# Kernel tuning notes

Hardware: AMD Instinct MI355X
Metric: run time of the kernel (lower is better)

## Reference

```python
import jax, jax.numpy as jnp
import numpy as np

A = 9  # len(scales) * len(ratios) anchor templates
DN = ('NHWC', 'HWIO', 'NHWC')


def _conv(x, w, b):
    y = jax.lax.conv_general_dilated(x, w, window_strides=(1, 1), padding='SAME',
                                     dimension_numbers=DN)
    return y + b


def setup_inputs() -> dict:
    key = jax.random.key(0)
    ks = jax.random.split(key, 9)
    s = 0.02  # weight init scale
    x = jax.random.normal(ks[0], (4, 128, 128, 512), jnp.float32)
    W1 = jax.random.normal(ks[1], (3, 3, 512, 256), jnp.float32) * s
    b1 = jnp.zeros((256,), jnp.float32)
    W2 = jax.random.normal(ks[2], (3, 3, 256, 256), jnp.float32) * s
    b2 = jnp.zeros((256,), jnp.float32)
    Wr = jax.random.normal(ks[3], (1, 1, 256, 4 * A), jnp.float32) * s
    br = jnp.zeros((4 * A,), jnp.float32)
    Wc = jax.random.normal(ks[4], (1, 1, 256, 2 * A), jnp.float32) * s
    bc = jnp.zeros((2 * A,), jnp.float32)
    return {'x': x, 'W1': W1, 'b1': b1, 'W2': W2, 'b2': b2,
            'Wr': Wr, 'br': br, 'Wc': Wc, 'bc': bc}


def reference(x, W1, b1, W2, b2, Wr, br, Wc, bc):
    h = jax.nn.relu(_conv(x, W1, b1))
    h = jax.nn.relu(_conv(h, W2, b2))
    B, H, W = h.shape[0], h.shape[1], h.shape[2]
    reg = _conv(h, Wr, br).reshape(B, H, W, A, 4)            # (B,H,W,A,4)
    cls = _conv(h, Wc, bc).reshape(B, H, W, A, 2)            # (B,H,W,A,2)
    cls = jax.nn.softmax(cls, axis=4)
    return jnp.concatenate((cls, reg), axis=4)               # (B,H,W,A,6)
```

## Files before the change

kernel.cpp:

```cpp
#include <hip/hip_runtime.h>


typedef float f32x4  __attribute__((ext_vector_type(4)));
typedef float f32x16 __attribute__((ext_vector_type(16)));
typedef short bf16x8 __attribute__((ext_vector_type(8)));

union U16x8 { uint4 v; unsigned short s[8]; };

__device__ __forceinline__ unsigned short f2bf(float f) {
  union { float f; unsigned int u; } v; v.f = f;
  unsigned int r = v.u + 0x7FFFu + ((v.u >> 16) & 1u);
  return (unsigned short)(r >> 16);
}

#define GLOAD_LDS16(G, L)                                        \
  __builtin_amdgcn_global_load_lds(                              \
      (const __attribute__((address_space(1))) void*)(G),        \
      (__attribute__((address_space(3))) void*)(L), 16, 0, 0)

__global__ __launch_bounds__(256) void transpose_cvt(
    const float* __restrict__ src, unsigned short* __restrict__ dst,
    int K, int N) {
  __shared__ float t[32][33];
  const int tx = threadIdx.x, ty = threadIdx.y;
  const int k0 = blockIdx.x * 32, n0 = blockIdx.y * 32;
  const float* s = src + (size_t)blockIdx.z * K * N;
  unsigned short* d = dst + (size_t)blockIdx.z * N * K;
#pragma unroll
  for (int r = 0; r < 32; r += 8) {
    int k = k0 + ty + r, n = n0 + tx;
    t[ty + r][tx] = (k < K && n < N) ? s[(size_t)k * N + n] : 0.f;
  }
  __syncthreads();
#pragma unroll
  for (int r = 0; r < 32; r += 8) {
    int n = n0 + ty + r, k = k0 + tx;
    if (n < N && k < K) d[(size_t)n * K + k] = f2bf(t[tx][ty + r]);
  }
}

__global__ __launch_bounds__(256) void convert_x(
    const float* __restrict__ x, unsigned short* __restrict__ xp) {
  int idx = blockIdx.x * 256 + threadIdx.x;
  int g = idx & 63;
  int cell = idx >> 6;
  int xpix = cell % 130;
  int t = cell / 130;
  int ypix = t % 130;
  int b = t / 130;
  U16x8 u;
  if (xpix == 0 || xpix == 129 || ypix == 0 || ypix == 129) {
    u.v = make_uint4(0u, 0u, 0u, 0u);
  } else {
    const float* sp = x + ((size_t)((b * 128 + ypix - 1) * 128) + (xpix - 1)) * 512 + g * 8;
    float4 a = *(const float4*)sp;
    float4 c = *(const float4*)(sp + 4);
    u.s[0] = f2bf(a.x); u.s[1] = f2bf(a.y); u.s[2] = f2bf(a.z); u.s[3] = f2bf(a.w);
    u.s[4] = f2bf(c.x); u.s[5] = f2bf(c.y); u.s[6] = f2bf(c.z); u.s[7] = f2bf(c.w);
  }
  *(uint4*)(xp + (size_t)cell * 512 + g * 8) = u.v;
}

__global__ __launch_bounds__(256) void zero_h1_borders(unsigned short* __restrict__ h1p) {
  int idx = blockIdx.x * 256 + threadIdx.x;
  int g = idx & 31;
  int cell = idx >> 5;
  int xpix = cell % 130;
  int t = cell / 130;
  int ypix = t % 130;
  if (xpix == 0 || xpix == 129 || ypix == 0 || ypix == 129)
    *(uint4*)(h1p + (size_t)cell * 256 + g * 8) = make_uint4(0u, 0u, 0u, 0u);
}

template<int CIN, int MODE>
__global__ __launch_bounds__(512, 2) void conv3x3(
    const unsigned short* __restrict__ Ap,
    const unsigned short* __restrict__ WT,
    const float* __restrict__ bias,
    unsigned short* __restrict__ out) {
  constexpr int NCI    = CIN / 32;
  constexpr int LOGNCI = (NCI == 16) ? 4 : 3;
  constexpr int NT     = 3 * NCI;
  constexpr int A_BYTES = 2 * 192 * 4 * 16;
  constexpr int B_BYTES = 3 * 256 * 4 * 16;
  constexpr int BUF     = A_BYTES + B_BYTES;
  __shared__ __align__(16) unsigned char smem[2 * BUF];

  const int tid  = threadIdx.x;
  const int wave = tid >> 6, lane = tid & 63;
  const int l31 = lane & 31, hi = lane >> 5;
  const int wm = wave >> 2, wn = wave & 3;
  const int b = blockIdx.x >> 6;
  const int y0 = (blockIdx.x & 63) * 2;
  const int brow = b * 130 + y0;

  int a_go[3], a_ld[3];
#pragma unroll
  for (int i = 0; i < 3; ++i) {
    int s = (wave * 3 + i) * 64 + lane;
    int br = (s >= 768) ? 1 : 0;
    int r = s - br * 768;
    int px = r >> 2, sl = r & 3;
    a_go[i] = (br * 130 + px) * CIN + ((sl ^ ((px >> 1) & 3)) * 8);
    a_ld[i] = (wave * 3 + i) * 1024;
  }
  int b_go[6], b_ld[6];
#pragma unroll
  for (int i = 0; i < 6; ++i) {
    int s = (wave * 6 + i) * 64 + lane;
    int dxs = s >> 10, r = s & 1023;
    int co = r >> 2, sl = r & 3;
    b_go[i] = (dxs * 256 + co) * CIN + ((sl ^ ((co >> 1) & 3)) * 8);
    b_ld[i] = A_BYTES + (wave * 6 + i) * 1024;
  }

  const float bb0 = bias[wn * 64 + l31];
  const float bb1 = bias[wn * 64 + 32 + l31];

  f32x16 acc[4][2] = {};
  const int bswz = (l31 >> 1) & 3;

  auto stage = [&](int tile) {
    const int dy  = tile >> LOGNCI;
    const int ci0 = (tile & (NCI - 1)) << 5;
    unsigned char* sb = smem + (size_t)(tile & 1) * BUF;
    const unsigned short* Ab = Ap + (size_t)(brow + dy) * 130 * CIN + ci0;
#pragma unroll
    for (int i = 0; i < 3; ++i)
      GLOAD_LDS16(Ab + a_go[i], sb + a_ld[i]);
    const unsigned short* Bb = WT + (size_t)dy * 3 * 256 * CIN + ci0;
#pragma unroll
    for (int i = 0; i < 6; ++i)
      GLOAD_LDS16(Bb + b_go[i], sb + b_ld[i]);
  };

  stage(0);
  asm volatile("s_waitcnt vmcnt(0)" ::: "memory");
  __builtin_amdgcn_s_barrier();

#pragma unroll 2
  for (int t = 0; t < NT; ++t) {
    const unsigned char* sb = smem + (size_t)(t & 1) * BUF;
#pragma unroll
    for (int dx = 0; dx < 3; ++dx) {
      const int aswz  = ((l31 + dx) >> 1) & 3;
      const int abase = wm * 12288 + (l31 + dx) * 64;
      const int bbase = A_BYTES + dx * 16384 + wn * 4096 + l31 * 64;
      bf16x8 af[2][4], bfr[2][2];
#pragma unroll
      for (int ks = 0; ks < 2; ++ks) {
        const int q  = ks * 2 + hi;
        const int ab  = abase + ((q ^ aswz) * 16);
        const int bby = bbase + ((q ^ bswz) * 16);
#pragma unroll
        for (int i = 0; i < 4; ++i)
          af[ks][i] = *(const bf16x8*)(sb + ab + i * 2048);
#pragma unroll
        for (int j = 0; j < 2; ++j)
          bfr[ks][j] = *(const bf16x8*)(sb + bby + j * 2048);
      }
      if (dx == 0 && t + 1 < NT) stage(t + 1);
      if (dx == 2 && t + 1 < NT)
        asm volatile("s_waitcnt vmcnt(0)" ::: "memory");
      __builtin_amdgcn_sched_barrier(0);
      __builtin_amdgcn_s_barrier();
      asm volatile("s_waitcnt lgkmcnt(0)" ::: "memory");
      __builtin_amdgcn_sched_barrier(0);
      __builtin_amdgcn_s_setprio(1);
#pragma unroll
      for (int ks = 0; ks < 2; ++ks)
#pragma unroll
        for (int i = 0; i < 4; ++i)
#pragma unroll
          for (int j = 0; j < 2; ++j)
            acc[i][j] = __builtin_amdgcn_mfma_f32_32x32x16_bf16(
                af[ks][i], bfr[ks][j], acc[i][j], 0, 0, 0);
      __builtin_amdgcn_s_setprio(0);
      __builtin_amdgcn_sched_barrier(0);
      __builtin_amdgcn_s_barrier();
    }
  }

#pragma unroll
  for (int i = 0; i < 4; ++i) {
#pragma unroll
    for (int j = 0; j < 2; ++j) {
      const int n = wn * 64 + j * 32 + l31;
      const float bb = j ? bb1 : bb0;
#pragma unroll
      for (int reg = 0; reg < 16; ++reg) {
        int px = i * 32 + (reg & 3) + 8 * (reg >> 2) + 4 * hi;
        float v = fmaxf(acc[i][j][reg] + bb, 0.f);
        size_t off;
        if (MODE == 0)
          off = ((size_t)(brow + wm + 1) * 130 + (px + 1)) * 256 + n;
        else
          off = ((size_t)(b * 128 + y0 + wm) * 128 + px) * 256 + n;
        out[off] = f2bf(v);
      }
    }
  }
}

__global__ __launch_bounds__(256) void heads_kernel(
    const unsigned short* __restrict__ h2,
    const unsigned short* __restrict__ WhT,
    const float* __restrict__ br, const float* __restrict__ bc,
    float* __restrict__ out) {
  __shared__ __align__(16) unsigned short As[64][264];
  const int tid = threadIdx.x;
  const int wave = tid >> 6, lane = tid & 63;
  const int quad = lane >> 4, l16 = lane & 15;
  const int pix0 = blockIdx.x * 64;
#pragma unroll
  for (int r = 0; r < 8; ++r) {
    int s = r * 256 + tid;
    int row = s >> 5, seg = s & 31;
    *(uint4*)&As[row][seg * 8] =
        *(const uint4*)(h2 + (size_t)(pix0 + row) * 256 + seg * 8);
  }
  __syncthreads();
  f32x4 acc[4] = {};
#pragma unroll
  for (int ks = 0; ks < 8; ++ks) {
    bf16x8 af = *(const bf16x8*)&As[wave * 16 + l16][ks * 32 + quad * 8];
#pragma unroll
    for (int j = 0; j < 4; ++j) {
      bf16x8 bfr = *(const bf16x8*)(WhT + (size_t)(j * 16 + l16) * 256 + ks * 32 + quad * 8);
      acc[j] = __builtin_amdgcn_mfma_f32_16x16x32_bf16(af, bfr, acc[j], 0, 0, 0);
    }
  }
#pragma unroll
  for (int j = 0; j < 4; ++j) {
    int n = j * 16 + l16;
    float bias = 0.f;
    if (n < 18) bias = bc[n];
    else if (n < 54) bias = br[n - 18];
#pragma unroll
    for (int r = 0; r < 4; ++r) {
      int p = pix0 + wave * 16 + quad * 4 + r;
      float v = acc[j][r] + bias;
      float partner = __shfl_xor(v, 1);
      if (n < 18) {
        float mx = fmaxf(v, partner);
        float e0 = __expf(v - mx), e1 = __expf(partner - mx);
        int a = n >> 1, sl = n & 1;
        out[(size_t)p * 54 + a * 6 + sl] = e0 / (e0 + e1);
      } else if (n < 54) {
        int rr = n - 18, a = rr >> 2, sl = (rr & 3) + 2;
        out[(size_t)p * 54 + a * 6 + sl] = v;
      }
    }
  }
}

extern "C" void kernel_launch(void* const* d_in, const int* in_sizes, int n_in,
                              void* d_out, int out_size, void* d_ws, size_t ws_size,
                              hipStream_t stream) {
  const float* x  = (const float*)d_in[0];
  const float* W1 = (const float*)d_in[1];
  const float* b1 = (const float*)d_in[2];
  const float* W2 = (const float*)d_in[3];
  const float* b2 = (const float*)d_in[4];
  const float* Wr = (const float*)d_in[5];
  const float* br = (const float*)d_in[6];
  const float* Wc = (const float*)d_in[7];
  const float* bc = (const float*)d_in[8];
  float* out = (float*)d_out;

  constexpr size_t XPAD_B  = 4ull * 130 * 130 * 512 * 2;
  constexpr size_t H1PAD_B = 4ull * 130 * 130 * 256 * 2;
  constexpr size_t H2_B    = 4ull * 128 * 128 * 256 * 2;
  constexpr size_t W1T_B   = 9ull * 256 * 512 * 2;
  constexpr size_t W2T_B   = 9ull * 256 * 256 * 2;
  char* ws = (char*)d_ws;
  unsigned short* x_pad  = (unsigned short*)(ws);
  unsigned short* h1_pad = (unsigned short*)(ws + XPAD_B);
  unsigned short* h2     = (unsigned short*)(ws + XPAD_B + H1PAD_B);
  unsigned short* W1T    = (unsigned short*)(ws + XPAD_B + H1PAD_B + H2_B);
  unsigned short* W2T    = (unsigned short*)(ws + XPAD_B + H1PAD_B + H2_B + W1T_B);
  unsigned short* WhT    = (unsigned short*)(ws + XPAD_B + H1PAD_B + H2_B + W1T_B + W2T_B);

  hipMemsetAsync(WhT, 0, 64ull * 256 * 2, stream);
  transpose_cvt<<<dim3(16, 8, 9), dim3(32, 8), 0, stream>>>(W1, W1T, 512, 256);
  transpose_cvt<<<dim3(8, 8, 9),  dim3(32, 8), 0, stream>>>(W2, W2T, 256, 256);
  transpose_cvt<<<dim3(8, 1, 1),  dim3(32, 8), 0, stream>>>(Wc, WhT, 256, 18);
  transpose_cvt<<<dim3(8, 2, 1),  dim3(32, 8), 0, stream>>>(Wr, WhT + 18 * 256, 256, 36);
  convert_x<<<16900, 256, 0, stream>>>(x, x_pad);
  zero_h1_borders<<<8450, 256, 0, stream>>>(h1_pad);
  conv3x3<512, 0><<<256, 512, 0, stream>>>(x_pad, W1T, b1, h1_pad);
  conv3x3<256, 1><<<256, 512, 0, stream>>>(h1_pad, W2T, b2, h2);
  heads_kernel<<<1024, 256, 0, stream>>>(h2, WhT, br, bc, out);
}
```

Measured before the change: 481.5 us.

## Halve conv workgroup to 4 waves with 128x128 tiles and register-double-buffered fragments

The conv kernel now runs 4 waves per block instead of 8, so each wave owns a 128x128 output tile (16 accumulators) rather than 128x64. This raises MFMA work per LDS fragment load. LDS fragment loads are double-buffered in registers (X/Y sets) and overlapped with MFMAs using partial lgkmcnt waits, and the per-dx barriers are replaced by one barrier per k-tile. In exchange, each wave carries much higher register pressure (256 accumulator floats plus fragments), launch_bounds(256,1) limits occupancy, and each thread issues twice as many global-to-LDS copies.

```diff
diff --git a/kernel.cpp b/kernel.cpp
--- a/kernel.cpp
+++ b/kernel.cpp
@@ -73,7 +73,7 @@
 }
 
 template<int CIN, int MODE>
-__global__ __launch_bounds__(512, 2) void conv3x3(
+__global__ __launch_bounds__(256, 1) void conv3x3(
     const unsigned short* __restrict__ Ap,
     const unsigned short* __restrict__ WT,
     const float* __restrict__ bias,
@@ -89,35 +89,29 @@
   const int tid  = threadIdx.x;
   const int wave = tid >> 6, lane = tid & 63;
   const int l31 = lane & 31, hi = lane >> 5;
-  const int wm = wave >> 2, wn = wave & 3;
+  const int wm = wave >> 1, wn = wave & 1;
   const int b = blockIdx.x >> 6;
   const int y0 = (blockIdx.x & 63) * 2;
   const int brow = b * 130 + y0;
 
-  int a_go[3], a_ld[3];
-#pragma unroll
-  for (int i = 0; i < 3; ++i) {
-    int s = (wave * 3 + i) * 64 + lane;
-    int br = (s >= 768) ? 1 : 0;
-    int r = s - br * 768;
-    int px = r >> 2, sl = r & 3;
-    a_go[i] = (br * 130 + px) * CIN + ((sl ^ ((px >> 1) & 3)) * 8);
-    a_ld[i] = (wave * 3 + i) * 1024;
-  }
-  int b_go[6], b_ld[6];
+  int a_go[6], b_go[12];
 #pragma unroll
   for (int i = 0; i < 6; ++i) {
     int s = (wave * 6 + i) * 64 + lane;
+    int rw = (s >= 768) ? 1 : 0;
+    int r = s - rw * 768;
+    int px = r >> 2, sl = r & 3;
+    a_go[i] = (rw * 130 + px) * CIN + ((sl ^ ((px >> 1) & 3)) * 8);
+  }
+#pragma unroll
+  for (int i = 0; i < 12; ++i) {
+    int s = (wave * 12 + i) * 64 + lane;
     int dxs = s >> 10, r = s & 1023;
     int co = r >> 2, sl = r & 3;
     b_go[i] = (dxs * 256 + co) * CIN + ((sl ^ ((co >> 1) & 3)) * 8);
-    b_ld[i] = A_BYTES + (wave * 6 + i) * 1024;
-  }
-
-  const float bb0 = bias[wn * 64 + l31];
-  const float bb1 = bias[wn * 64 + 32 + l31];
-
-  f32x16 acc[4][2] = {};
+  }
+
+  f32x16 acc[4][4] = {};
   const int bswz = (l31 >> 1) & 3;
 
   auto stage = [&](int tile) {
@@ -126,67 +120,94 @@
     unsigned char* sb = smem + (size_t)(tile & 1) * BUF;
     const unsigned short* Ab = Ap + (size_t)(brow + dy) * 130 * CIN + ci0;
 #pragma unroll
-    for (int i = 0; i < 3; ++i)
-      GLOAD_LDS16(Ab + a_go[i], sb + a_ld[i]);
+    for (int i = 0; i < 6; ++i)
+      GLOAD_LDS16(Ab + a_go[i], sb + (wave * 6 + i) * 1024);
     const unsigned short* Bb = WT + (size_t)dy * 3 * 256 * CIN + ci0;
 #pragma unroll
-    for (int i = 0; i < 6; ++i)
-      GLOAD_LDS16(Bb + b_go[i], sb + b_ld[i]);
+    for (int i = 0; i < 12; ++i)
+      GLOAD_LDS16(Bb + b_go[i], sb + A_BYTES + (wave * 12 + i) * 1024);
   };
+
+  bf16x8 Xa0, Xa1, Xa2, Xa3, Xb0, Xb1, Xb2, Xb3;
+  bf16x8 Ya0, Ya1, Ya2, Ya3, Yb0, Yb1, Yb2, Yb3;
+
+#define LOAD_FRAGS(SB, P, DX, KS) do {                                        \
+    const unsigned char* sb_ = (SB);                                          \
+    const int q_  = (KS) * 2 + hi;                                            \
+    const int ab_ = wm * 12288 + (l31 + (DX)) * 64 +                          \
+                    ((q_ ^ (((l31 + (DX)) >> 1) & 3)) * 16);                  \
+    P##a0 = *(const bf16x8*)(sb_ + ab_);                                      \
+    P##a1 = *(const bf16x8*)(sb_ + ab_ + 2048);                               \
+    P##a2 = *(const bf16x8*)(sb_ + ab_ + 4096);                               \
+    P##a3 = *(const bf16x8*)(sb_ + ab_ + 6144);                               \
+    const int bb_ = A_BYTES + (DX) * 16384 + wn * 8192 + l31 * 64 +           \
+                    ((q_ ^ bswz) * 16);                                       \
+    P##b0 = *(const bf16x8*)(sb_ + bb_);                                      \
+    P##b1 = *(const bf16x8*)(sb_ + bb_ + 2048);                               \
+    P##b2 = *(const bf16x8*)(sb_ + bb_ + 4096);                               \
+    P##b3 = *(const bf16x8*)(sb_ + bb_ + 6144);                               \
+  } while (0)
+
+#define MFMA_SET(P) do {                                                      \
+    acc[0][0] = __builtin_amdgcn_mfma_f32_32x32x16_bf16(P##a0, P##b0, acc[0][0], 0, 0, 0); \
+    acc[1][0] = __builtin_amdgcn_mfma_f32_32x32x16_bf16(P##a1, P##b0, acc[1][0], 0, 0, 0); \
+    acc[2][0] = __builtin_amdgcn_mfma_f32_32x32x16_bf16(P##a2, P##b0, acc[2][0], 0, 0, 0); \
+    acc[3][0] = __builtin_amdgcn_mfma_f32_32x32x16_bf16(P##a3, P##b0, acc[3][0], 0, 0, 0); \
+    acc[0][1] = __builtin_amdgcn_mfma_f32_32x32x16_bf16(P##a0, P##b1, acc[0][1], 0, 0, 0); \
+    acc[1][1] = __builtin_amdgcn_mfma_f32_32x32x16_bf16(P##a1, P##b1, acc[1][1], 0, 0, 0); \
+    acc[2][1] = __builtin_amdgcn_mfma_f32_32x32x16_bf16(P##a2, P##b1, acc[2][1], 0, 0, 0); \
+    acc[3][1] = __builtin_amdgcn_mfma_f32_32x32x16_bf16(P##a3, P##b1, acc[3][1], 0, 0, 0); \
+    acc[0][2] = __builtin_amdgcn_mfma_f32_32x32x16_bf16(P##a0, P##b2, acc[0][2], 0, 0, 0); \
+    acc[1][2] = __builtin_amdgcn_mfma_f32_32x32x16_bf16(P##a1, P##b2, acc[1][2], 0, 0, 0); \
+    acc[2][2] = __builtin_amdgcn_mfma_f32_32x32x16_bf16(P##a2, P##b2, acc[2][2], 0, 0, 0); \
+    acc[3][2] = __builtin_amdgcn_mfma_f32_32x32x16_bf16(P##a3, P##b2, acc[3][2], 0, 0, 0); \
+    acc[0][3] = __builtin_amdgcn_mfma_f32_32x32x16_bf16(P##a0, P##b3, acc[0][3], 0, 0, 0); \
+    acc[1][3] = __builtin_amdgcn_mfma_f32_32x32x16_bf16(P##a1, P##b3, acc[1][3], 0, 0, 0); \
+    acc[2][3] = __builtin_amdgcn_mfma_f32_32x32x16_bf16(P##a2, P##b3, acc[2][3], 0, 0, 0); \
+    acc[3][3] = __builtin_amdgcn_mfma_f32_32x32x16_bf16(P##a3, P##b3, acc[3][3], 0, 0, 0); \
+  } while (0)
+
+#define W8 do { asm volatile("s_waitcnt lgkmcnt(8)" ::: "memory");            \
+                __builtin_amdgcn_sched_barrier(0); } while (0)
+#define W0 do { asm volatile("s_waitcnt lgkmcnt(0)" ::: "memory");            \
+                __builtin_amdgcn_sched_barrier(0); } while (0)
 
   stage(0);
   asm volatile("s_waitcnt vmcnt(0)" ::: "memory");
   __builtin_amdgcn_s_barrier();
-
-#pragma unroll 2
+  LOAD_FRAGS(smem, Y, 0, 0);
+
+#pragma unroll 1
   for (int t = 0; t < NT; ++t) {
-    const unsigned char* sb = smem + (size_t)(t & 1) * BUF;
-#pragma unroll
-    for (int dx = 0; dx < 3; ++dx) {
-      const int aswz  = ((l31 + dx) >> 1) & 3;
-      const int abase = wm * 12288 + (l31 + dx) * 64;
-      const int bbase = A_BYTES + dx * 16384 + wn * 4096 + l31 * 64;
-      bf16x8 af[2][4], bfr[2][2];
-#pragma unroll
-      for (int ks = 0; ks < 2; ++ks) {
-        const int q  = ks * 2 + hi;
-        const int ab  = abase + ((q ^ aswz) * 16);
-        const int bby = bbase + ((q ^ bswz) * 16);
-#pragma unroll
-        for (int i = 0; i < 4; ++i)
-          af[ks][i] = *(const bf16x8*)(sb + ab + i * 2048);
-#pragma unroll
-        for (int j = 0; j < 2; ++j)
-          bfr[ks][j] = *(const bf16x8*)(sb + bby + j * 2048);
-      }
-      if (dx == 0 && t + 1 < NT) stage(t + 1);
-      if (dx == 2 && t + 1 < NT)
-        asm volatile("s_waitcnt vmcnt(0)" ::: "memory");
-      __builtin_amdgcn_sched_barrier(0);
-      __builtin_amdgcn_s_barrier();
-      asm volatile("s_waitcnt lgkmcnt(0)" ::: "memory");
-      __builtin_amdgcn_sched_barrier(0);
-      __builtin_amdgcn_s_setprio(1);
-#pragma unroll
-      for (int ks = 0; ks < 2; ++ks)
-#pragma unroll
-        for (int i = 0; i < 4; ++i)
-#pragma unroll
-          for (int j = 0; j < 2; ++j)
-            acc[i][j] = __builtin_amdgcn_mfma_f32_32x32x16_bf16(
-                af[ks][i], bfr[ks][j], acc[i][j], 0, 0, 0);
-      __builtin_amdgcn_s_setprio(0);
-      __builtin_amdgcn_sched_barrier(0);
-      __builtin_amdgcn_s_barrier();
+    const unsigned char* sb  = smem + (size_t)(t & 1) * BUF;
+    const unsigned char* sbn = smem + (size_t)((t + 1) & 1) * BUF;
+    if (t + 1 < NT) stage(t + 1);
+    LOAD_FRAGS(sb, X, 0, 1); W8; MFMA_SET(Y);
+    LOAD_FRAGS(sb, Y, 1, 0); W8; MFMA_SET(X);
+    LOAD_FRAGS(sb, X, 1, 1); W8; MFMA_SET(Y);
+    LOAD_FRAGS(sb, Y, 2, 0); W8; MFMA_SET(X);
+    asm volatile("s_waitcnt vmcnt(0)" ::: "memory");
+    __builtin_amdgcn_s_barrier();
+    LOAD_FRAGS(sb, X, 2, 1); W8; MFMA_SET(Y);
+    if (t + 1 < NT) {
+      LOAD_FRAGS(sbn, Y, 0, 0); W8; MFMA_SET(X);
+    } else {
+      W0; MFMA_SET(X);
     }
-  }
-
-#pragma unroll
-  for (int i = 0; i < 4; ++i) {
-#pragma unroll
-    for (int j = 0; j < 2; ++j) {
-      const int n = wn * 64 + j * 32 + l31;
-      const float bb = j ? bb1 : bb0;
+    __builtin_amdgcn_s_barrier();
+  }
+
+#undef LOAD_FRAGS
+#undef MFMA_SET
+#undef W8
+#undef W0
+
+#pragma unroll
+  for (int j = 0; j < 4; ++j) {
+    const int n = wn * 128 + j * 32 + l31;
+    const float bb = bias[n];
+#pragma unroll
+    for (int i = 0; i < 4; ++i) {
 #pragma unroll
       for (int reg = 0; reg < 16; ++reg) {
         int px = i * 32 + (reg & 3) + 8 * (reg >> 2) + 4 * hi;
@@ -195,7 +216,7 @@
         if (MODE == 0)
           off = ((size_t)(brow + wm + 1) * 130 + (px + 1)) * 256 + n;
         else
-          off = ((size_t)(b * 128 + y0 + wm) * 128 + px) * 256 + n;
+          off = ((size_t)((b * 128 + y0 + wm) * 128) + px) * 256 + n;
         out[off] = f2bf(v);
       }
     }
@@ -288,7 +309,7 @@
   transpose_cvt<<<dim3(8, 2, 1),  dim3(32, 8), 0, stream>>>(Wr, WhT + 18 * 256, 256, 36);
   convert_x<<<16900, 256, 0, stream>>>(x, x_pad);
   zero_h1_borders<<<8450, 256, 0, stream>>>(h1_pad);
-  conv3x3<512, 0><<<256, 512, 0, stream>>>(x_pad, W1T, b1, h1_pad);
-  conv3x3<256, 1><<<256, 512, 0, stream>>>(h1_pad, W2T, b2, h2);
+  conv3x3<512, 0><<<256, 256, 0, stream>>>(x_pad, W1T, b1, h1_pad);
+  conv3x3<256, 1><<<256, 256, 0, stream>>>(h1_pad, W2T, b2, h2);
   heads_kernel<<<1024, 256, 0, stream>>>(h2, WhT, br, bc, out);
 }
```

Measured after the change: 1.608 ms. 3.34x slower.
